# Optimization experiments

Hardware: AMD Instinct MI355X
Metric: run time of the kernel (lower is better)

The kernel has to match this reference:

```python
import jax, jax.numpy as jnp
import numpy as np

B, S = 64, 256
VOCAB, DL, DA, DV = 30522, 300, 74, 35
DH, GH, LH, RH = 128, 64, 128, 128  # modality dim, proj-GRU hidden, LSTM hidden, RGN hidden


def _gru_dir(x, Wi, Wh, bi, bh):
    # x: [B,S,D] -> [B,S,H]; torch GRU gate order (r, z, n)
    xg = x @ Wi + bi  # [B,S,3H] precomputed input projections
    H = Wh.shape[0]
    def step(h, xg_t):
        hg = h @ Wh + bh
        xr, xz, xn = jnp.split(xg_t, 3, axis=-1)
        hr, hz, hn = jnp.split(hg, 3, axis=-1)
        r = jax.nn.sigmoid(xr + hr)
        z = jax.nn.sigmoid(xz + hz)
        n = jnp.tanh(xn + r * hn)
        h = (1.0 - z) * n + z * h
        return h, h
    h0 = jnp.zeros((x.shape[0], H), x.dtype)
    _, ys = jax.lax.scan(step, h0, jnp.swapaxes(xg, 0, 1))
    return jnp.swapaxes(ys, 0, 1)


def _bigru(x, Wi, Wh, bi, bh):
    f = _gru_dir(x, Wi[0], Wh[0], bi[0], bh[0])
    b = _gru_dir(x[:, ::-1], Wi[1], Wh[1], bi[1], bh[1])[:, ::-1]
    return jnp.concatenate([f, b], axis=-1)


def _lstm_dir(x, Wi, Wh, bi, bh):
    xg = x @ Wi + bi  # [B,S,4H]; torch LSTM gate order (i, f, g, o)
    H = Wh.shape[0]
    def step(carry, xg_t):
        h, c = carry
        g = xg_t + h @ Wh + bh
        i, f, gg, o = jnp.split(g, 4, axis=-1)
        c = jax.nn.sigmoid(f) * c + jax.nn.sigmoid(i) * jnp.tanh(gg)
        h = jax.nn.sigmoid(o) * jnp.tanh(c)
        return (h, c), h
    z = jnp.zeros((x.shape[0], H), x.dtype)
    _, ys = jax.lax.scan(step, (z, z), jnp.swapaxes(xg, 0, 1))
    return jnp.swapaxes(ys, 0, 1)


def _bilstm(x, Wi, Wh, bi, bh):
    f = _lstm_dir(x, Wi[0], Wh[0], bi[0], bh[0])
    b = _lstm_dir(x[:, ::-1], Wi[1], Wh[1], bi[1], bh[1])[:, ::-1]
    return jnp.concatenate([f, b], axis=-1)


def _rgn_scan(x, h0, Wx, Wh, b):
    # RGNCell: gated recurrent cell (GRU-style), returns final state [B,H]
    xg = x @ Wx + b  # [B,S,3H]
    def step(h, xg_t):
        hg = h @ Wh
        xr, xz, xn = jnp.split(xg_t, 3, axis=-1)
        hr, hz, hn = jnp.split(hg, 3, axis=-1)
        r = jax.nn.sigmoid(xr + hr)
        z = jax.nn.sigmoid(xz + hz)
        n = jnp.tanh(xn + r * hn)
        return (1.0 - z) * n + z * h, None
    h, _ = jax.lax.scan(step, h0, jnp.swapaxes(xg, 0, 1))
    return h


def _xattn(q, kv):
    # parameter-free scaled dot-product cross-modal attention (JCAF)
    scale = 1.0 / np.sqrt(q.shape[-1]).astype(np.float32)
    s = jnp.einsum('bsd,btd->bst', q, kv) * scale
    return jnp.einsum('bst,btd->bsd', jax.nn.softmax(s, axis=-1), kv)


def _forward(sentences, acoustic, video, state0, state1, emb,
             proj_l_W, proj_l_b, proj_a_W, proj_a_b, proj_v_W, proj_v_b,
             gru_Wi, gru_Wh, gru_bi, gru_bh,
             lstm_Wi, lstm_Wh, lstm_bi, lstm_bh,
             rgn_Wx, rgn_Wh, rgn_b, fc1_W, fc1_b, fc2_W, fc2_b):
    enc = emb[sentences]                          # LanguageEmbeddingLayer: [B,S,DL]
    # SeqEncoder: project each modality to 128-d (dropout off in eval)
    seq_l = enc @ proj_l_W + proj_l_b             # [B,S,128]
    seq_a = acoustic @ proj_a_W + proj_a_b
    seq_v = video @ proj_v_W + proj_v_b
    # project_l/a/v: bidirectional GRU 128 -> 2*64 = 128
    x_l = _bigru(seq_l, gru_Wi[0], gru_Wh[0], gru_bi[0], gru_bh[0])
    x_a = _bigru(seq_a, gru_Wi[1], gru_Wh[1], gru_bi[1], gru_bh[1])
    x_v = _bigru(seq_v, gru_Wi[2], gru_Wh[2], gru_bi[2], gru_bh[2])
    # JCAF: each modality enriched by cross-attention to the other two
    fin_txt = x_l + _xattn(x_l, x_a) + _xattn(x_l, x_v)
    fin_aud = x_a + _xattn(x_a, x_l) + _xattn(x_a, x_v)
    fin_vis = x_v + _xattn(x_v, x_l) + _xattn(x_v, x_a)
    tstep = jnp.concatenate([fin_txt, fin_aud, fin_vis], axis=-1)      # [B,S,384]
    step_fusion = _bilstm(tstep, lstm_Wi, lstm_Wh, lstm_bi, lstm_bh)   # [B,S,256]
    # two custom RGNCell recurrences: forward sweep + reversed sweep
    out0 = _rgn_scan(step_fusion, state0, rgn_Wx[0], rgn_Wh[0], rgn_b[0])
    out1 = _rgn_scan(step_fusion[:, ::-1], state1, rgn_Wx[1], rgn_Wh[1], rgn_b[1])
    h = jax.nn.leaky_relu((out0 + out1) @ fc1_W + fc1_b)
    return h @ fc2_W + fc2_b                     # [B,1]


def setup_inputs():
    keys = iter(jax.random.split(jax.random.key(0), 48))
    def rn(shape, s=0.05):
        return jax.random.normal(next(keys), shape, jnp.float32) * s
    return {
        'sentences': jax.random.randint(next(keys), (B, S), 0, VOCAB),
        'acoustic': jax.random.normal(next(keys), (B, S, DA), jnp.float32),
        'video': jax.random.normal(next(keys), (B, S, DV), jnp.float32),
        'state0': jax.random.normal(next(keys), (B, RH), jnp.float32),
        'state1': jax.random.normal(next(keys), (B, RH), jnp.float32),
        'emb': rn((VOCAB, DL), 0.1),
        'proj_l_W': rn((DL, DH)), 'proj_l_b': rn((DH,)),
        'proj_a_W': rn((DA, DH)), 'proj_a_b': rn((DH,)),
        'proj_v_W': rn((DV, DH)), 'proj_v_b': rn((DH,)),
        'gru_Wi': rn((3, 2, DH, 3 * GH)), 'gru_Wh': rn((3, 2, GH, 3 * GH)),
        'gru_bi': rn((3, 2, 3 * GH)), 'gru_bh': rn((3, 2, 3 * GH)),
        'lstm_Wi': rn((2, 3 * DH, 4 * LH)), 'lstm_Wh': rn((2, LH, 4 * LH)),
        'lstm_bi': rn((2, 4 * LH)), 'lstm_bh': rn((2, 4 * LH)),
        'rgn_Wx': rn((2, 2 * LH, 3 * RH)), 'rgn_Wh': rn((2, RH, 3 * RH)),
        'rgn_b': rn((2, 3 * RH)),
        'fc1_W': rn((RH, 32)), 'fc1_b': rn((32,)),
        'fc2_W': rn((32, 1)), 'fc2_b': rn((1,)),
    }


def reference(sentences, acoustic, video, state0, state1, emb,
              proj_l_W, proj_l_b, proj_a_W, proj_a_b, proj_v_W, proj_v_b,
              gru_Wi, gru_Wh, gru_bi, gru_bh,
              lstm_Wi, lstm_Wh, lstm_bi, lstm_bh,
              rgn_Wx, rgn_Wh, rgn_b, fc1_W, fc1_b, fc2_W, fc2_b):
    return _forward(sentences, acoustic, video, state0, state1, emb,
                    proj_l_W, proj_l_b, proj_a_W, proj_a_b, proj_v_W, proj_v_b,
                    gru_Wi, gru_Wh, gru_bi, gru_bh,
                    lstm_Wi, lstm_Wh, lstm_bi, lstm_bh,
                    rgn_Wx, rgn_Wh, rgn_b, fc1_W, fc1_b, fc2_W, fc2_b)
```

## Files before the change

### kernel.cpp

```cpp
#include <hip/hip_runtime.h>

#define WS_SEQ      0LL
#define WS_XGGRU    6291456LL
#define WS_X        0LL
#define WS_TSTEP    18874368LL
#define WS_S        6291456LL
#define WS_XGLSTM   0LL
#define WS_SF       16777216LL
#define WS_XGRGN    0LL
#define WS_OUT0     20971520LL

__device__ __forceinline__ float sigf(float x) {
    return __builtin_amdgcn_rcpf(1.f + __expf(-x));
}
__device__ __forceinline__ float tanhfast(float x) {
    float e = __expf(2.f * x);
    return 1.f - 2.f * __builtin_amdgcn_rcpf(e + 1.f);
}
__device__ __forceinline__ float rl(float v, int i) {
    return __int_as_float(__builtin_amdgcn_readlane(__float_as_int(v), i));
}

typedef float vf16 __attribute__((ext_vector_type(16)));

#define LD16(V, P, S) { _Pragma("unroll") \
    for (int _j = 0; _j < 16; ++_j) (V)[_j] = (P)[_j * (S)]; }
#define DOT16(ACC, V, H, B) { _Pragma("unroll") \
    for (int _j = 0; _j < 16; ++_j) (ACC) = fmaf(rl((H), (B) + _j), (V)[_j], (ACC)); }

__device__ __forceinline__ void gemm_body(
    const float* __restrict__ Ab, int lda, const int* __restrict__ idx,
    const float* __restrict__ Wb, int wld, int wtrans,
    const float* __restrict__ bb,
    float* __restrict__ Cb, int ldc,
    int K, float alpha, int accum)
{
    int m0 = blockIdx.y * 64, n0 = blockIdx.x * 64;
    int t = threadIdx.x;
    int tx = t & 7, ty = t >> 3;

    __shared__ __align__(16) float As[16][68];
    __shared__ __align__(16) float Ws[16][68];

    float acc[8][8];
#pragma unroll
    for (int i = 0; i < 8; ++i)
#pragma unroll
        for (int j = 0; j < 8; ++j) acc[i][j] = 0.f;

    long long arow[4];
#pragma unroll
    for (int i = 0; i < 4; ++i) {
        int m = (t + i * 64) >> 2;
        arow[i] = idx ? (long long)idx[m0 + m] : (long long)(m0 + m);
    }
    const bool a_vec = ((lda & 3) == 0);

    for (int k0 = 0; k0 < K; k0 += 16) {
#pragma unroll
        for (int i = 0; i < 4; ++i) {
            int j = t + i * 64;
            int m = j >> 2, kq = j & 3;
            int kk = k0 + kq * 4;
            const float* p = Ab + arow[i] * (long long)lda + kk;
            float4 v = {0.f, 0.f, 0.f, 0.f};
            if (a_vec && kk + 3 < K) {
                v = *(const float4*)p;
            } else {
                if (kk + 0 < K) v.x = p[0];
                if (kk + 1 < K) v.y = p[1];
                if (kk + 2 < K) v.z = p[2];
                if (kk + 3 < K) v.w = p[3];
            }
            As[kq * 4 + 0][m] = v.x; As[kq * 4 + 1][m] = v.y;
            As[kq * 4 + 2][m] = v.z; As[kq * 4 + 3][m] = v.w;
        }
        if (!wtrans) {
#pragma unroll
            for (int i = 0; i < 4; ++i) {
                int j = t + i * 64;
                int k = j >> 4, nq = j & 15;
                float4 v = {0.f, 0.f, 0.f, 0.f};
                if (k0 + k < K)
                    v = *(const float4*)(Wb + (long long)(k0 + k) * wld + n0 + nq * 4);
                *(float4*)&Ws[k][nq * 4] = v;
            }
        } else {
#pragma unroll
            for (int i = 0; i < 4; ++i) {
                int j = t + i * 64;
                int n = j >> 2, kq = j & 3;
                int kk = k0 + kq * 4;
                const float* p = Wb + (long long)(n0 + n) * wld + kk;
                float4 v = {0.f, 0.f, 0.f, 0.f};
                if (kk + 3 < K) v = *(const float4*)p;
                else {
                    if (kk + 0 < K) v.x = p[0];
                    if (kk + 1 < K) v.y = p[1];
                    if (kk + 2 < K) v.z = p[2];
                    if (kk + 3 < K) v.w = p[3];
                }
                Ws[kq * 4 + 0][n] = v.x; Ws[kq * 4 + 1][n] = v.y;
                Ws[kq * 4 + 2][n] = v.z; Ws[kq * 4 + 3][n] = v.w;
            }
        }
        __syncthreads();
#pragma unroll
        for (int k = 0; k < 16; ++k) {
            float4 a0 = *(const float4*)&As[k][ty * 8];
            float4 a1 = *(const float4*)&As[k][ty * 8 + 4];
            float4 b0 = *(const float4*)&Ws[k][tx * 8];
            float4 b1 = *(const float4*)&Ws[k][tx * 8 + 4];
            float av[8] = {a0.x, a0.y, a0.z, a0.w, a1.x, a1.y, a1.z, a1.w};
            float bv[8] = {b0.x, b0.y, b0.z, b0.w, b1.x, b1.y, b1.z, b1.w};
#pragma unroll
            for (int i = 0; i < 8; ++i)
#pragma unroll
                for (int j = 0; j < 8; ++j)
                    acc[i][j] = fmaf(av[i], bv[j], acc[i][j]);
        }
        __syncthreads();
    }

#pragma unroll
    for (int i = 0; i < 8; ++i) {
        long long gm = m0 + ty * 8 + i;
#pragma unroll
        for (int jq = 0; jq < 2; ++jq) {
            float* cp = Cb + gm * ldc + n0 + tx * 8 + jq * 4;
            float4 v;
            v.x = alpha * acc[i][jq * 4 + 0]; v.y = alpha * acc[i][jq * 4 + 1];
            v.z = alpha * acc[i][jq * 4 + 2]; v.w = alpha * acc[i][jq * 4 + 3];
            if (bb) {
                const float* bp = bb + n0 + tx * 8 + jq * 4;
                v.x += bp[0]; v.y += bp[1]; v.z += bp[2]; v.w += bp[3];
            }
            if (accum) {
                float4 o = *(const float4*)cp;
                v.x += o.x; v.y += o.y; v.z += o.z; v.w += o.w;
            }
            *(float4*)cp = v;
        }
    }
}

__global__ __launch_bounds__(64) void gemm_k(
    const float* __restrict__ A, long long a_z, int a_zdiv, int lda,
    const int* __restrict__ idx,
    const float* __restrict__ W, long long w_z, int wld, int wtrans,
    const float* __restrict__ bias, int bias_z,
    float* __restrict__ C, long long c_z, int ldc,
    int K, float alpha, int accum)
{
    int z = blockIdx.z;
    gemm_body(A + (long long)(z / a_zdiv) * a_z, lda, idx,
              W + (long long)z * w_z, wld, wtrans,
              bias ? bias + (long long)z * bias_z : nullptr,
              C + (long long)z * c_z, ldc, K, alpha, accum);
}

__global__ __launch_bounds__(64) void att_score_k(
    const float* __restrict__ X, float* __restrict__ S,
    int q0, int q1, int q2, int k0, int k1, int k2)
{
    int z = blockIdx.z;
    int pair = z >> 6, b = z & 63;
    int qi = pair == 0 ? q0 : (pair == 1 ? q1 : q2);
    int ki = pair == 0 ? k0 : (pair == 1 ? k1 : k2);
    gemm_body(X + (long long)qi * 2097152 + (long long)b * 32768, 128, nullptr,
              X + (long long)ki * 2097152 + (long long)b * 32768, 128, 1,
              nullptr,
              S + (long long)z * 65536, 256, 128, 0.08838834764831845f, 0);
}

__global__ __launch_bounds__(64) void att_apply_k(
    const float* __restrict__ S, const float* __restrict__ X,
    float* __restrict__ tstep,
    int q0, int q1, int q2, int k0, int k1, int k2)
{
    int z = blockIdx.z;
    int pair = z >> 6, b = z & 63;
    int qi = pair == 0 ? q0 : (pair == 1 ? q1 : q2);
    int ki = pair == 0 ? k0 : (pair == 1 ? k1 : k2);
    gemm_body(S + (long long)z * 65536, 256, nullptr,
              X + (long long)ki * 2097152 + (long long)b * 32768, 128, 0,
              nullptr,
              tstep + (long long)qi * 128 + (long long)b * 98304, 384,
              256, 1.f, 1);
}

__global__ __launch_bounds__(256) void copy_tstep_k(const float* __restrict__ x,
                                                    float* __restrict__ tstep)
{
    int o = blockIdx.x * 256 + threadIdx.x;
    int c = o % 384;
    int row = o / 384;
    int m = c >> 7, cc = c & 127;
    tstep[o] = x[(long long)m * 2097152 + (long long)row * 128 + cc];
}

__global__ __launch_bounds__(256) void softmax_k(float* __restrict__ S)
{
    int wave = threadIdx.x >> 6, lane = threadIdx.x & 63;
    int row = blockIdx.x * 4 + wave;
    float* p = S + (long long)row * 256;
    float v[4];
    float mx = -1e30f;
#pragma unroll
    for (int i = 0; i < 4; ++i) { v[i] = p[lane + i * 64]; mx = fmaxf(mx, v[i]); }
#pragma unroll
    for (int off = 32; off > 0; off >>= 1) mx = fmaxf(mx, __shfl_xor(mx, off));
    float sum = 0.f;
#pragma unroll
    for (int i = 0; i < 4; ++i) { v[i] = __expf(v[i] - mx); sum += v[i]; }
#pragma unroll
    for (int off = 32; off > 0; off >>= 1) sum += __shfl_xor(sum, off);
    float inv = 1.f / sum;
#pragma unroll
    for (int i = 0; i < 4; ++i) p[lane + i * 64] = v[i] * inv;
}

__global__ __launch_bounds__(192) void gru_rec_k(const float* __restrict__ xg,
                                                 const float* __restrict__ Wh,
                                                 const float* __restrict__ bh,
                                                 float* __restrict__ xout)
{
    int b = blockIdx.x, z = blockIdx.y;
    int m = z >> 1, d = z & 1;
    int tid = threadIdx.x, lane = tid & 63;
    int c = tid;
    const float* Whz = Wh + (long long)z * 12288;
    const float* wp = Whz + c;
    vf16 W0, W1, W2, W3;
    LD16(W0, wp + 0 * 16 * 192, 192); LD16(W1, wp + 1 * 16 * 192, 192);
    LD16(W2, wp + 2 * 16 * 192, 192); LD16(W3, wp + 3 * 16 * 192, 192);
    float bias = bh[z * 192 + c];

    __shared__ float g[2][192];
    int n = lane;
    float h = 0.f;
    const float* xgb = xg + (long long)z * 3145728 + (long long)b * 49152;
    float* xob = xout + (long long)m * 2097152 + (long long)b * 32768 + d * 64;
    int tt0 = d ? 255 : 0;
    const float* xr0 = xgb + tt0 * 192;
    float x_r = xr0[n], x_z = xr0[64 + n], x_n = xr0[128 + n];

#pragma unroll 1
    for (int t = 0; t < 256; ++t) {
        int tt = d ? 255 - t : t;
        float nx_r = 0, nx_z = 0, nx_n = 0;
        if (t < 255) {
            const float* xr = xgb + (d ? tt - 1 : tt + 1) * 192;
            nx_r = xr[n]; nx_z = xr[64 + n]; nx_n = xr[128 + n];
        }
        float s0 = bias, s1 = 0.f, s2 = 0.f, s3 = 0.f;
        DOT16(s0, W0, h, 0);  DOT16(s1, W1, h, 16);
        DOT16(s2, W2, h, 32); DOT16(s3, W3, h, 48);
        g[t & 1][c] = (s0 + s1) + (s2 + s3);
        __syncthreads();
        const float* gp = g[t & 1];
        float r  = sigf(x_r + gp[n]);
        float zz = sigf(x_z + gp[64 + n]);
        float nn = tanhfast(x_n + r * gp[128 + n]);
        h = (1.f - zz) * nn + zz * h;
        if (c < 64) xob[tt * 128 + n] = h;
        x_r = nx_r; x_z = nx_z; x_n = nx_n;
    }
}

__global__ __launch_bounds__(1024) void lstm_rec_k(const float* __restrict__ xg,
                                                   const float* __restrict__ Wh,
                                                   const float* __restrict__ bh,
                                                   float* __restrict__ sf)
{
    int b = blockIdx.x, d = blockIdx.y;
    int tid = threadIdx.x, lane = tid & 63;
    int kh = tid >> 9;
    int c  = tid & 511;
    const float* Whz = Wh + (long long)d * 65536;
    const float* wp = Whz + (long long)(kh * 64) * 512 + c;
    vf16 W0, W1, W2, W3;
    LD16(W0, wp + 0 * 16 * 512, 512); LD16(W1, wp + 1 * 16 * 512, 512);
    LD16(W2, wp + 2 * 16 * 512, 512); LD16(W3, wp + 3 * 16 * 512, 512);

    __shared__ float part[2][1024];
    int n = kh * 64 + lane;
    float h = 0.f, cst = 0.f;
    const float* xgb = xg + (long long)d * 8388608 + (long long)b * 131072;
    float* sfb = sf + (long long)b * 65536 + d * 128;

    float bias = 0.f, xc = 0.f;
    if (kh == 0) {
        bias = bh[d * 512 + c];
        int tt0 = d ? 255 : 0;
        xc = xgb[tt0 * 512 + c];
    }

#pragma unroll 1
    for (int t = 0; t < 256; ++t) {
        int tt = d ? 255 - t : t;
        float nxc = 0.f;
        if (kh == 0 && t < 255)
            nxc = xgb[(d ? tt - 1 : tt + 1) * 512 + c];
        float s0 = xc + bias, s1 = 0.f, s2 = 0.f, s3 = 0.f;
        DOT16(s0, W0, h, 0);  DOT16(s1, W1, h, 16);
        DOT16(s2, W2, h, 32); DOT16(s3, W3, h, 48);
        part[t & 1][kh * 512 + c] = (s0 + s1) + (s2 + s3);
        __syncthreads();
        const float* p = part[t & 1];
        float iv = p[n]       + p[512 + n];
        float fv = p[128 + n] + p[512 + 128 + n];
        float gv = p[256 + n] + p[512 + 256 + n];
        float ov = p[384 + n] + p[512 + 384 + n];
        cst = sigf(fv) * cst + sigf(iv) * tanhfast(gv);
        h = sigf(ov) * tanhfast(cst);
        if (c < 64) sfb[tt * 256 + n] = h;
        xc = nxc;
    }
}

__global__ __launch_bounds__(768) void rgn_rec_k(const float* __restrict__ xg,
                                                 const float* __restrict__ Wh,
                                                 const float* __restrict__ state0,
                                                 const float* __restrict__ state1,
                                                 float* __restrict__ outbase)
{
    int b = blockIdx.x, d = blockIdx.y;
    int tid = threadIdx.x, lane = tid & 63;
    int kh = (tid >= 384) ? 1 : 0;
    int c  = tid - kh * 384;
    const float* Whz = Wh + (long long)d * 49152;
    const float* wp = Whz + (long long)(kh * 64) * 384 + c;
    vf16 W0, W1, W2, W3;
    LD16(W0, wp + 0 * 16 * 384, 384); LD16(W1, wp + 1 * 16 * 384, 384);
    LD16(W2, wp + 2 * 16 * 384, 384); LD16(W3, wp + 3 * 16 * 384, 384);

    __shared__ float part[2][768];
    int n = kh * 64 + lane;
    const float* st = d ? state1 : state0;
    float h = st[b * 128 + n];
    const float* xgb = xg + (long long)d * 6291456 + (long long)b * 98304;
    int tt0 = d ? 255 : 0;
    const float* xr0 = xgb + tt0 * 384;
    float x_r = xr0[n], x_z = xr0[128 + n], x_n = xr0[256 + n];

#pragma unroll 1
    for (int t = 0; t < 256; ++t) {
        int tt = d ? 255 - t : t;
        float nx_r = 0, nx_z = 0, nx_n = 0;
        if (t < 255) {
            const float* xr = xgb + (d ? tt - 1 : tt + 1) * 384;
            nx_r = xr[n]; nx_z = xr[128 + n]; nx_n = xr[256 + n];
        }
        float s0 = 0.f, s1 = 0.f, s2 = 0.f, s3 = 0.f;
        DOT16(s0, W0, h, 0);  DOT16(s1, W1, h, 16);
        DOT16(s2, W2, h, 32); DOT16(s3, W3, h, 48);
        part[t & 1][kh * 384 + c] = (s0 + s1) + (s2 + s3);
        __syncthreads();
        const float* p = part[t & 1];
        float pr = p[n]       + p[384 + n];
        float pz = p[128 + n] + p[384 + 128 + n];
        float pn = p[256 + n] + p[384 + 256 + n];
        float r  = sigf(x_r + pr);
        float zz = sigf(x_z + pz);
        float nn = tanhfast(x_n + r * pn);
        h = (1.f - zz) * nn + zz * h;
        x_r = nx_r; x_z = nx_z; x_n = nx_n;
    }
    if (c < 64) outbase[(long long)d * 8192 + b * 128 + n] = h;
}

__global__ __launch_bounds__(256) void fc_k(const float* __restrict__ o01,
                                            const float* __restrict__ f1W,
                                            const float* __restrict__ f1b,
                                            const float* __restrict__ f2W,
                                            const float* __restrict__ f2b,
                                            float* __restrict__ out)
{
    __shared__ float s[8192];
    __shared__ float h1[2048];
    int tid = threadIdx.x;
    for (int e = tid; e < 8192; e += 256) s[e] = o01[e] + o01[8192 + e];
    __syncthreads();
    for (int o = tid; o < 2048; o += 256) {
        int b = o >> 5, q = o & 31;
        float acc = f1b[q];
        for (int k = 0; k < 128; ++k) acc += s[b * 128 + k] * f1W[k * 32 + q];
        h1[o] = acc >= 0.f ? acc : 0.01f * acc;
    }
    __syncthreads();
    if (tid < 64) {
        float acc = f2b[0];
        for (int q = 0; q < 32; ++q) acc += h1[tid * 32 + q] * f2W[q];
        out[tid] = acc;
    }
}

extern "C" void kernel_launch(void* const* d_in, const int* in_sizes, int n_in,
                              void* d_out, int out_size, void* d_ws, size_t ws_size,
                              hipStream_t stream)
{
    const int*   sent     = (const int*)  d_in[0];
    const float* acoustic = (const float*)d_in[1];
    const float* video    = (const float*)d_in[2];
    const float* state0   = (const float*)d_in[3];
    const float* state1   = (const float*)d_in[4];
    const float* emb      = (const float*)d_in[5];
    const float* plW = (const float*)d_in[6],  *plb = (const float*)d_in[7];
    const float* paW = (const float*)d_in[8],  *pab = (const float*)d_in[9];
    const float* pvW = (const float*)d_in[10], *pvb = (const float*)d_in[11];
    const float* gWi = (const float*)d_in[12], *gWh = (const float*)d_in[13];
    const float* gbi = (const float*)d_in[14], *gbh = (const float*)d_in[15];
    const float* lWi = (const float*)d_in[16], *lWh = (const float*)d_in[17];
    const float* lbi = (const float*)d_in[18], *lbh = (const float*)d_in[19];
    const float* rWx = (const float*)d_in[20], *rWh = (const float*)d_in[21];
    const float* rb  = (const float*)d_in[22];
    const float* f1W = (const float*)d_in[23], *f1b = (const float*)d_in[24];
    const float* f2W = (const float*)d_in[25], *f2b = (const float*)d_in[26];
    float* ws  = (float*)d_ws;
    float* out = (float*)d_out;

    dim3 blk(64);

    gemm_k<<<dim3(2, 256, 1), blk, 0, stream>>>(emb, 0, 1, 300, sent,
        plW, 0, 128, 0, plb, 0, ws + WS_SEQ, 0, 128, 300, 1.f, 0);
    gemm_k<<<dim3(2, 256, 1), blk, 0, stream>>>(acoustic, 0, 1, 74, nullptr,
        paW, 0, 128, 0, pab, 0, ws + WS_SEQ + 2097152, 0, 128, 74, 1.f, 0);
    gemm_k<<<dim3(2, 256, 1), blk, 0, stream>>>(video, 0, 1, 35, nullptr,
        pvW, 0, 128, 0, pvb, 0, ws + WS_SEQ + 4194304, 0, 128, 35, 1.f, 0);

    gemm_k<<<dim3(3, 256, 6), blk, 0, stream>>>(ws + WS_SEQ, 2097152, 2, 128, nullptr,
        gWi, 24576, 192, 0, gbi, 192, ws + WS_XGGRU, 3145728, 192, 128, 1.f, 0);

    gru_rec_k<<<dim3(64, 6), dim3(192), 0, stream>>>(ws + WS_XGGRU, gWh, gbh, ws + WS_X);

    copy_tstep_k<<<dim3(24576), dim3(256), 0, stream>>>(ws + WS_X, ws + WS_TSTEP);

    att_score_k<<<dim3(4, 4, 192), blk, 0, stream>>>(ws + WS_X, ws + WS_S,
        0, 1, 2, 1, 0, 0);
    softmax_k<<<dim3(12288), dim3(256), 0, stream>>>(ws + WS_S);
    att_apply_k<<<dim3(2, 4, 192), blk, 0, stream>>>(ws + WS_S, ws + WS_X,
        ws + WS_TSTEP, 0, 1, 2, 1, 0, 0);
    att_score_k<<<dim3(4, 4, 192), blk, 0, stream>>>(ws + WS_X, ws + WS_S,
        0, 1, 2, 2, 2, 1);
    softmax_k<<<dim3(12288), dim3(256), 0, stream>>>(ws + WS_S);
    att_apply_k<<<dim3(2, 4, 192), blk, 0, stream>>>(ws + WS_S, ws + WS_X,
        ws + WS_TSTEP, 0, 1, 2, 2, 2, 1);

    gemm_k<<<dim3(8, 256, 2), blk, 0, stream>>>(ws + WS_TSTEP, 0, 1, 384, nullptr,
        lWi, 196608, 512, 0, lbi, 512, ws + WS_XGLSTM, 8388608, 512, 384, 1.f, 0);

    lstm_rec_k<<<dim3(64, 2), dim3(1024), 0, stream>>>(ws + WS_XGLSTM, lWh, lbh, ws + WS_SF);

    gemm_k<<<dim3(6, 256, 2), blk, 0, stream>>>(ws + WS_SF, 0, 1, 256, nullptr,
        rWx, 98304, 384, 0, rb, 384, ws + WS_XGRGN, 6291456, 384, 256, 1.f, 0);

    rgn_rec_k<<<dim3(64, 2), dim3(768), 0, stream>>>(ws + WS_XGRGN, rWh, state0, state1,
                                                     ws + WS_OUT0);

    fc_k<<<dim3(1), dim3(256), 0, stream>>>(ws + WS_OUT0, f1W, f1b, f2W, f2b, out);
}
```

Baseline: 1.654 ms.

## Use packed FP32 FMA in recurrent kernels with two output columns per thread

The GRU, LSTM and RGN recurrence kernels now give each thread two adjacent gate columns. They hold the weights as 64 float2 registers and run the hidden-state matvec with inline-asm v_pk_fma_f32, using readlane-broadcast hidden values placed in hardcoded SGPR pairs. Block sizes are halved (192→128, 1024→512, 768→384), which cuts the number of waves and FMA instructions per serial timestep. The cost is extra readlane and s_mov instructions plus hand-pinned scalar registers. In the GRU, part of a wave now sits idle during the matvec.

```diff
diff --git a/kernel.cpp b/kernel.cpp
--- a/kernel.cpp
+++ b/kernel.cpp
@@ -17,16 +17,46 @@
     float e = __expf(2.f * x);
     return 1.f - 2.f * __builtin_amdgcn_rcpf(e + 1.f);
 }
-__device__ __forceinline__ float rl(float v, int i) {
-    return __int_as_float(__builtin_amdgcn_readlane(__float_as_int(v), i));
-}
-
-typedef float vf16 __attribute__((ext_vector_type(16)));
-
-#define LD16(V, P, S) { _Pragma("unroll") \
-    for (int _j = 0; _j < 16; ++_j) (V)[_j] = (P)[_j * (S)]; }
-#define DOT16(ACC, V, H, B) { _Pragma("unroll") \
-    for (int _j = 0; _j < 16; ++_j) (ACC) = fmaf(rl((H), (B) + _j), (V)[_j], (ACC)); }
+
+typedef float vf2 __attribute__((ext_vector_type(2)));
+
+#define LDW64(W, P, S) { _Pragma("unroll") \
+    for (int _k = 0; _k < 64; ++_k) (W)[_k] = *(const vf2*)((P) + _k * (S)); }
+
+#define PK4(A0, A1, Wa, Wb, Wc, Wd, H, K0, K1, K2, K3) \
+  asm("v_readlane_b32 s60, %6, " #K0 "\n\t" \
+      "v_readlane_b32 s62, %6, " #K1 "\n\t" \
+      "v_readlane_b32 s64, %6, " #K2 "\n\t" \
+      "v_readlane_b32 s66, %6, " #K3 "\n\t" \
+      "s_mov_b32 s61, s60\n\t" \
+      "s_mov_b32 s63, s62\n\t" \
+      "s_mov_b32 s65, s64\n\t" \
+      "s_mov_b32 s67, s66\n\t" \
+      "v_pk_fma_f32 %0, %2, s[60:61], %0\n\t" \
+      "v_pk_fma_f32 %1, %3, s[62:63], %1\n\t" \
+      "v_pk_fma_f32 %0, %4, s[64:65], %0\n\t" \
+      "v_pk_fma_f32 %1, %5, s[66:67], %1" \
+      : "+v"(A0), "+v"(A1) \
+      : "v"(Wa), "v"(Wb), "v"(Wc), "v"(Wd), "v"(H) \
+      : "s60","s61","s62","s63","s64","s65","s66","s67");
+
+#define PKALL(A0, A1, W, H) \
+  PK4(A0,A1,W[0],W[1],W[2],W[3],H,0,1,2,3) \
+  PK4(A0,A1,W[4],W[5],W[6],W[7],H,4,5,6,7) \
+  PK4(A0,A1,W[8],W[9],W[10],W[11],H,8,9,10,11) \
+  PK4(A0,A1,W[12],W[13],W[14],W[15],H,12,13,14,15) \
+  PK4(A0,A1,W[16],W[17],W[18],W[19],H,16,17,18,19) \
+  PK4(A0,A1,W[20],W[21],W[22],W[23],H,20,21,22,23) \
+  PK4(A0,A1,W[24],W[25],W[26],W[27],H,24,25,26,27) \
+  PK4(A0,A1,W[28],W[29],W[30],W[31],H,28,29,30,31) \
+  PK4(A0,A1,W[32],W[33],W[34],W[35],H,32,33,34,35) \
+  PK4(A0,A1,W[36],W[37],W[38],W[39],H,36,37,38,39) \
+  PK4(A0,A1,W[40],W[41],W[42],W[43],H,40,41,42,43) \
+  PK4(A0,A1,W[44],W[45],W[46],W[47],H,44,45,46,47) \
+  PK4(A0,A1,W[48],W[49],W[50],W[51],H,48,49,50,51) \
+  PK4(A0,A1,W[52],W[53],W[54],W[55],H,52,53,54,55) \
+  PK4(A0,A1,W[56],W[57],W[58],W[59],H,56,57,58,59) \
+  PK4(A0,A1,W[60],W[61],W[62],W[63],H,60,61,62,63)
 
 __device__ __forceinline__ void gemm_body(
     const float* __restrict__ Ab, int lda, const int* __restrict__ idx,
@@ -220,7 +250,7 @@
     for (int i = 0; i < 4; ++i) p[lane + i * 64] = v[i] * inv;
 }
 
-__global__ __launch_bounds__(192) void gru_rec_k(const float* __restrict__ xg,
+__global__ __launch_bounds__(128) void gru_rec_k(const float* __restrict__ xg,
                                                  const float* __restrict__ Wh,
                                                  const float* __restrict__ bh,
                                                  float* __restrict__ xout)
@@ -228,13 +258,14 @@
     int b = blockIdx.x, z = blockIdx.y;
     int m = z >> 1, d = z & 1;
     int tid = threadIdx.x, lane = tid & 63;
-    int c = tid;
+    int cp = tid;
+    int act = cp < 96;
+    int cpc = act ? cp : 0;
     const float* Whz = Wh + (long long)z * 12288;
-    const float* wp = Whz + c;
-    vf16 W0, W1, W2, W3;
-    LD16(W0, wp + 0 * 16 * 192, 192); LD16(W1, wp + 1 * 16 * 192, 192);
-    LD16(W2, wp + 2 * 16 * 192, 192); LD16(W3, wp + 3 * 16 * 192, 192);
-    float bias = bh[z * 192 + c];
+    const float* wp = Whz + 2 * cpc;
+    vf2 Wk[64];
+    LDW64(Wk, wp, 192);
+    vf2 bias2 = *(const vf2*)(bh + z * 192 + 2 * cpc);
 
     __shared__ float g[2][192];
     int n = lane;
@@ -253,35 +284,33 @@
             const float* xr = xgb + (d ? tt - 1 : tt + 1) * 192;
             nx_r = xr[n]; nx_z = xr[64 + n]; nx_n = xr[128 + n];
         }
-        float s0 = bias, s1 = 0.f, s2 = 0.f, s3 = 0.f;
-        DOT16(s0, W0, h, 0);  DOT16(s1, W1, h, 16);
-        DOT16(s2, W2, h, 32); DOT16(s3, W3, h, 48);
-        g[t & 1][c] = (s0 + s1) + (s2 + s3);
+        vf2 a0 = bias2, a1 = {0.f, 0.f};
+        PKALL(a0, a1, Wk, h);
+        if (act) *(vf2*)&g[t & 1][2 * cp] = a0 + a1;
         __syncthreads();
         const float* gp = g[t & 1];
         float r  = sigf(x_r + gp[n]);
         float zz = sigf(x_z + gp[64 + n]);
         float nn = tanhfast(x_n + r * gp[128 + n]);
         h = (1.f - zz) * nn + zz * h;
-        if (c < 64) xob[tt * 128 + n] = h;
+        if (tid < 64) xob[tt * 128 + n] = h;
         x_r = nx_r; x_z = nx_z; x_n = nx_n;
     }
 }
 
-__global__ __launch_bounds__(1024) void lstm_rec_k(const float* __restrict__ xg,
-                                                   const float* __restrict__ Wh,
-                                                   const float* __restrict__ bh,
-                                                   float* __restrict__ sf)
+__global__ __launch_bounds__(512) void lstm_rec_k(const float* __restrict__ xg,
+                                                  const float* __restrict__ Wh,
+                                                  const float* __restrict__ bh,
+                                                  float* __restrict__ sf)
 {
     int b = blockIdx.x, d = blockIdx.y;
     int tid = threadIdx.x, lane = tid & 63;
-    int kh = tid >> 9;
-    int c  = tid & 511;
+    int kh = tid >> 8;
+    int cp = tid & 255;
     const float* Whz = Wh + (long long)d * 65536;
-    const float* wp = Whz + (long long)(kh * 64) * 512 + c;
-    vf16 W0, W1, W2, W3;
-    LD16(W0, wp + 0 * 16 * 512, 512); LD16(W1, wp + 1 * 16 * 512, 512);
-    LD16(W2, wp + 2 * 16 * 512, 512); LD16(W3, wp + 3 * 16 * 512, 512);
+    const float* wp = Whz + (long long)(kh * 64) * 512 + 2 * cp;
+    vf2 Wk[64];
+    LDW64(Wk, wp, 512);
 
     __shared__ float part[2][1024];
     int n = kh * 64 + lane;
@@ -289,23 +318,22 @@
     const float* xgb = xg + (long long)d * 8388608 + (long long)b * 131072;
     float* sfb = sf + (long long)b * 65536 + d * 128;
 
-    float bias = 0.f, xc = 0.f;
+    vf2 bias2 = {0.f, 0.f}, xc2 = {0.f, 0.f};
     if (kh == 0) {
-        bias = bh[d * 512 + c];
+        bias2 = *(const vf2*)(bh + d * 512 + 2 * cp);
         int tt0 = d ? 255 : 0;
-        xc = xgb[tt0 * 512 + c];
+        xc2 = *(const vf2*)(xgb + tt0 * 512 + 2 * cp);
     }
 
 #pragma unroll 1
     for (int t = 0; t < 256; ++t) {
         int tt = d ? 255 - t : t;
-        float nxc = 0.f;
+        vf2 nxc2 = {0.f, 0.f};
         if (kh == 0 && t < 255)
-            nxc = xgb[(d ? tt - 1 : tt + 1) * 512 + c];
-        float s0 = xc + bias, s1 = 0.f, s2 = 0.f, s3 = 0.f;
-        DOT16(s0, W0, h, 0);  DOT16(s1, W1, h, 16);
-        DOT16(s2, W2, h, 32); DOT16(s3, W3, h, 48);
-        part[t & 1][kh * 512 + c] = (s0 + s1) + (s2 + s3);
+            nxc2 = *(const vf2*)(xgb + (d ? tt - 1 : tt + 1) * 512 + 2 * cp);
+        vf2 a0 = xc2 + bias2, a1 = {0.f, 0.f};
+        PKALL(a0, a1, Wk, h);
+        *(vf2*)&part[t & 1][kh * 512 + 2 * cp] = a0 + a1;
         __syncthreads();
         const float* p = part[t & 1];
         float iv = p[n]       + p[512 + n];
@@ -314,12 +342,12 @@
         float ov = p[384 + n] + p[512 + 384 + n];
         cst = sigf(fv) * cst + sigf(iv) * tanhfast(gv);
         h = sigf(ov) * tanhfast(cst);
-        if (c < 64) sfb[tt * 256 + n] = h;
-        xc = nxc;
-    }
-}
-
-__global__ __launch_bounds__(768) void rgn_rec_k(const float* __restrict__ xg,
+        if (cp < 64) sfb[tt * 256 + n] = h;
+        xc2 = nxc2;
+    }
+}
+
+__global__ __launch_bounds__(384) void rgn_rec_k(const float* __restrict__ xg,
                                                  const float* __restrict__ Wh,
                                                  const float* __restrict__ state0,
                                                  const float* __restrict__ state1,
@@ -327,13 +355,12 @@
 {
     int b = blockIdx.x, d = blockIdx.y;
     int tid = threadIdx.x, lane = tid & 63;
-    int kh = (tid >= 384) ? 1 : 0;
-    int c  = tid - kh * 384;
+    int kh = (tid >= 192) ? 1 : 0;
+    int cp = tid - kh * 192;
     const float* Whz = Wh + (long long)d * 49152;
-    const float* wp = Whz + (long long)(kh * 64) * 384 + c;
-    vf16 W0, W1, W2, W3;
-    LD16(W0, wp + 0 * 16 * 384, 384); LD16(W1, wp + 1 * 16 * 384, 384);
-    LD16(W2, wp + 2 * 16 * 384, 384); LD16(W3, wp + 3 * 16 * 384, 384);
+    const float* wp = Whz + (long long)(kh * 64) * 384 + 2 * cp;
+    vf2 Wk[64];
+    LDW64(Wk, wp, 384);
 
     __shared__ float part[2][768];
     int n = kh * 64 + lane;
@@ -352,10 +379,9 @@
             const float* xr = xgb + (d ? tt - 1 : tt + 1) * 384;
             nx_r = xr[n]; nx_z = xr[128 + n]; nx_n = xr[256 + n];
         }
-        float s0 = 0.f, s1 = 0.f, s2 = 0.f, s3 = 0.f;
-        DOT16(s0, W0, h, 0);  DOT16(s1, W1, h, 16);
-        DOT16(s2, W2, h, 32); DOT16(s3, W3, h, 48);
-        part[t & 1][kh * 384 + c] = (s0 + s1) + (s2 + s3);
+        vf2 a0 = {0.f, 0.f}, a1 = {0.f, 0.f};
+        PKALL(a0, a1, Wk, h);
+        *(vf2*)&part[t & 1][kh * 384 + 2 * cp] = a0 + a1;
         __syncthreads();
         const float* p = part[t & 1];
         float pr = p[n]       + p[384 + n];
@@ -367,7 +393,7 @@
         h = (1.f - zz) * nn + zz * h;
         x_r = nx_r; x_z = nx_z; x_n = nx_n;
     }
-    if (c < 64) outbase[(long long)d * 8192 + b * 128 + n] = h;
+    if (cp < 64) outbase[(long long)d * 8192 + b * 128 + n] = h;
 }
 
 __global__ __launch_bounds__(256) void fc_k(const float* __restrict__ o01,
@@ -432,7 +458,7 @@
     gemm_k<<<dim3(3, 256, 6), blk, 0, stream>>>(ws + WS_SEQ, 2097152, 2, 128, nullptr,
         gWi, 24576, 192, 0, gbi, 192, ws + WS_XGGRU, 3145728, 192, 128, 1.f, 0);
 
-    gru_rec_k<<<dim3(64, 6), dim3(192), 0, stream>>>(ws + WS_XGGRU, gWh, gbh, ws + WS_X);
+    gru_rec_k<<<dim3(64, 6), dim3(128), 0, stream>>>(ws + WS_XGGRU, gWh, gbh, ws + WS_X);
 
     copy_tstep_k<<<dim3(24576), dim3(256), 0, stream>>>(ws + WS_X, ws + WS_TSTEP);
 
@@ -450,12 +476,12 @@
     gemm_k<<<dim3(8, 256, 2), blk, 0, stream>>>(ws + WS_TSTEP, 0, 1, 384, nullptr,
         lWi, 196608, 512, 0, lbi, 512, ws + WS_XGLSTM, 8388608, 512, 384, 1.f, 0);
 
-    lstm_rec_k<<<dim3(64, 2), dim3(1024), 0, stream>>>(ws + WS_XGLSTM, lWh, lbh, ws + WS_SF);
+    lstm_rec_k<<<dim3(64, 2), dim3(512), 0, stream>>>(ws + WS_XGLSTM, lWh, lbh, ws + WS_SF);
 
     gemm_k<<<dim3(6, 256, 2), blk, 0, stream>>>(ws + WS_SF, 0, 1, 256, nullptr,
         rWx, 98304, 384, 0, rb, 384, ws + WS_XGRGN, 6291456, 384, 256, 1.f, 0);
 
-    rgn_rec_k<<<dim3(64, 2), dim3(768), 0, stream>>>(ws + WS_XGRGN, rWh, state0, state1,
+    rgn_rec_k<<<dim3(64, 2), dim3(384), 0, stream>>>(ws + WS_XGRGN, rWh, state0, state1,
                                                      ws + WS_OUT0);
 
     fc_k<<<dim3(1), dim3(256), 0, stream>>>(ws + WS_OUT0, f1W, f1b, f2W, f2b, out);
```

Result: slower. 1.729 ms (+4.5%).

## Widen GEMM tiles to 64x128 with packed FMA and restructure LSTM recurrence

Applied to the files above, without the earlier changes.

The shared GEMM body now computes 64x128 output tiles per 64-thread block, accumulating with two-wide vector FMAs (packed FP32). A new N bound masks the partial column tiles, and launch bounds are tightened to one block. The LSTM recurrence kernel is halved to 512 threads, each handling two gate columns. Part of the recurrent weight matrix (36 rows) is staged in LDS, and the other 28 rows are read from global memory each step. This aims to cut register pressure and use packed math, at the cost of more accumulator registers in the GEMM and global weight traffic on every recurrence step.

```diff
diff --git a/kernel.cpp b/kernel.cpp
--- a/kernel.cpp
+++ b/kernel.cpp
@@ -22,6 +22,7 @@
 }
 
 typedef float vf16 __attribute__((ext_vector_type(16)));
+typedef float vf2 __attribute__((ext_vector_type(2)));
 
 #define LD16(V, P, S) { _Pragma("unroll") \
     for (int _j = 0; _j < 16; ++_j) (V)[_j] = (P)[_j * (S)]; }
@@ -33,20 +34,20 @@
     const float* __restrict__ Wb, int wld, int wtrans,
     const float* __restrict__ bb,
     float* __restrict__ Cb, int ldc,
-    int K, float alpha, int accum)
-{
-    int m0 = blockIdx.y * 64, n0 = blockIdx.x * 64;
+    int K, int N, float alpha, int accum)
+{
+    int m0 = blockIdx.y * 64, n0 = blockIdx.x * 128;
     int t = threadIdx.x;
     int tx = t & 7, ty = t >> 3;
 
     __shared__ __align__(16) float As[16][68];
-    __shared__ __align__(16) float Ws[16][68];
-
-    float acc[8][8];
+    __shared__ __align__(16) float Ws[16][132];
+
+    vf2 acc2[8][8];
 #pragma unroll
     for (int i = 0; i < 8; ++i)
 #pragma unroll
-        for (int j = 0; j < 8; ++j) acc[i][j] = 0.f;
+        for (int p = 0; p < 8; ++p) acc2[i][p] = (vf2){0.f, 0.f};
 
     long long arow[4];
 #pragma unroll
@@ -77,28 +78,31 @@
         }
         if (!wtrans) {
 #pragma unroll
-            for (int i = 0; i < 4; ++i) {
-                int j = t + i * 64;
-                int k = j >> 4, nq = j & 15;
+            for (int i = 0; i < 8; ++i) {
+                int q = t + i * 64;
+                int k = q >> 5, nq = q & 31;
+                int col = n0 + nq * 4;
                 float4 v = {0.f, 0.f, 0.f, 0.f};
-                if (k0 + k < K)
-                    v = *(const float4*)(Wb + (long long)(k0 + k) * wld + n0 + nq * 4);
+                if (k0 + k < K && col < N)
+                    v = *(const float4*)(Wb + (long long)(k0 + k) * wld + col);
                 *(float4*)&Ws[k][nq * 4] = v;
             }
         } else {
 #pragma unroll
-            for (int i = 0; i < 4; ++i) {
-                int j = t + i * 64;
-                int n = j >> 2, kq = j & 3;
+            for (int i = 0; i < 8; ++i) {
+                int q = t + i * 64;
+                int n = q >> 2, kq = q & 3;
                 int kk = k0 + kq * 4;
-                const float* p = Wb + (long long)(n0 + n) * wld + kk;
                 float4 v = {0.f, 0.f, 0.f, 0.f};
-                if (kk + 3 < K) v = *(const float4*)p;
-                else {
-                    if (kk + 0 < K) v.x = p[0];
-                    if (kk + 1 < K) v.y = p[1];
-                    if (kk + 2 < K) v.z = p[2];
-                    if (kk + 3 < K) v.w = p[3];
+                if (n0 + n < N) {
+                    const float* p = Wb + (long long)(n0 + n) * wld + kk;
+                    if (kk + 3 < K) v = *(const float4*)p;
+                    else {
+                        if (kk + 0 < K) v.x = p[0];
+                        if (kk + 1 < K) v.y = p[1];
+                        if (kk + 2 < K) v.z = p[2];
+                        if (kk + 3 < K) v.w = p[3];
+                    }
                 }
                 Ws[kq * 4 + 0][n] = v.x; Ws[kq * 4 + 1][n] = v.y;
                 Ws[kq * 4 + 2][n] = v.z; Ws[kq * 4 + 3][n] = v.w;
@@ -109,15 +113,23 @@
         for (int k = 0; k < 16; ++k) {
             float4 a0 = *(const float4*)&As[k][ty * 8];
             float4 a1 = *(const float4*)&As[k][ty * 8 + 4];
-            float4 b0 = *(const float4*)&Ws[k][tx * 8];
-            float4 b1 = *(const float4*)&Ws[k][tx * 8 + 4];
+            float4 b0 = *(const float4*)&Ws[k][tx * 4];
+            float4 b1 = *(const float4*)&Ws[k][32 + tx * 4];
+            float4 b2 = *(const float4*)&Ws[k][64 + tx * 4];
+            float4 b3 = *(const float4*)&Ws[k][96 + tx * 4];
             float av[8] = {a0.x, a0.y, a0.z, a0.w, a1.x, a1.y, a1.z, a1.w};
-            float bv[8] = {b0.x, b0.y, b0.z, b0.w, b1.x, b1.y, b1.z, b1.w};
-#pragma unroll
-            for (int i = 0; i < 8; ++i)
-#pragma unroll
-                for (int j = 0; j < 8; ++j)
-                    acc[i][j] = fmaf(av[i], bv[j], acc[i][j]);
+            vf2 bv[8];
+            bv[0] = (vf2){b0.x, b0.y}; bv[1] = (vf2){b0.z, b0.w};
+            bv[2] = (vf2){b1.x, b1.y}; bv[3] = (vf2){b1.z, b1.w};
+            bv[4] = (vf2){b2.x, b2.y}; bv[5] = (vf2){b2.z, b2.w};
+            bv[6] = (vf2){b3.x, b3.y}; bv[7] = (vf2){b3.z, b3.w};
+#pragma unroll
+            for (int i = 0; i < 8; ++i) {
+                vf2 a2 = {av[i], av[i]};
+#pragma unroll
+                for (int p = 0; p < 8; ++p)
+                    acc2[i][p] = __builtin_elementwise_fma(a2, bv[p], acc2[i][p]);
+            }
         }
         __syncthreads();
     }
@@ -126,40 +138,45 @@
     for (int i = 0; i < 8; ++i) {
         long long gm = m0 + ty * 8 + i;
 #pragma unroll
-        for (int jq = 0; jq < 2; ++jq) {
-            float* cp = Cb + gm * ldc + n0 + tx * 8 + jq * 4;
-            float4 v;
-            v.x = alpha * acc[i][jq * 4 + 0]; v.y = alpha * acc[i][jq * 4 + 1];
-            v.z = alpha * acc[i][jq * 4 + 2]; v.w = alpha * acc[i][jq * 4 + 3];
-            if (bb) {
-                const float* bp = bb + n0 + tx * 8 + jq * 4;
-                v.x += bp[0]; v.y += bp[1]; v.z += bp[2]; v.w += bp[3];
+        for (int jj = 0; jj < 4; ++jj) {
+            int col = n0 + jj * 32 + tx * 4;
+            if (col < N) {
+                float* cp = Cb + gm * ldc + col;
+                float4 v;
+                v.x = alpha * acc2[i][jj * 2 + 0][0];
+                v.y = alpha * acc2[i][jj * 2 + 0][1];
+                v.z = alpha * acc2[i][jj * 2 + 1][0];
+                v.w = alpha * acc2[i][jj * 2 + 1][1];
+                if (bb) {
+                    const float* bp = bb + col;
+                    v.x += bp[0]; v.y += bp[1]; v.z += bp[2]; v.w += bp[3];
+                }
+                if (accum) {
+                    float4 o = *(const float4*)cp;
+                    v.x += o.x; v.y += o.y; v.z += o.z; v.w += o.w;
+                }
+                *(float4*)cp = v;
             }
-            if (accum) {
-                float4 o = *(const float4*)cp;
-                v.x += o.x; v.y += o.y; v.z += o.z; v.w += o.w;
-            }
-            *(float4*)cp = v;
-        }
-    }
-}
-
-__global__ __launch_bounds__(64) void gemm_k(
+        }
+    }
+}
+
+__global__ __launch_bounds__(64, 1) void gemm_k(
     const float* __restrict__ A, long long a_z, int a_zdiv, int lda,
     const int* __restrict__ idx,
     const float* __restrict__ W, long long w_z, int wld, int wtrans,
     const float* __restrict__ bias, int bias_z,
     float* __restrict__ C, long long c_z, int ldc,
-    int K, float alpha, int accum)
+    int K, int N, float alpha, int accum)
 {
     int z = blockIdx.z;
     gemm_body(A + (long long)(z / a_zdiv) * a_z, lda, idx,
               W + (long long)z * w_z, wld, wtrans,
               bias ? bias + (long long)z * bias_z : nullptr,
-              C + (long long)z * c_z, ldc, K, alpha, accum);
-}
-
-__global__ __launch_bounds__(64) void att_score_k(
+              C + (long long)z * c_z, ldc, K, N, alpha, accum);
+}
+
+__global__ __launch_bounds__(64, 1) void att_score_k(
     const float* __restrict__ X, float* __restrict__ S,
     int q0, int q1, int q2, int k0, int k1, int k2)
 {
@@ -170,10 +187,10 @@
     gemm_body(X + (long long)qi * 2097152 + (long long)b * 32768, 128, nullptr,
               X + (long long)ki * 2097152 + (long long)b * 32768, 128, 1,
               nullptr,
-              S + (long long)z * 65536, 256, 128, 0.08838834764831845f, 0);
-}
-
-__global__ __launch_bounds__(64) void att_apply_k(
+              S + (long long)z * 65536, 256, 128, 256, 0.08838834764831845f, 0);
+}
+
+__global__ __launch_bounds__(64, 1) void att_apply_k(
     const float* __restrict__ S, const float* __restrict__ X,
     float* __restrict__ tstep,
     int q0, int q1, int q2, int k0, int k1, int k2)
@@ -186,7 +203,7 @@
               X + (long long)ki * 2097152 + (long long)b * 32768, 128, 0,
               nullptr,
               tstep + (long long)qi * 128 + (long long)b * 98304, 384,
-              256, 1.f, 1);
+              256, 128, 1.f, 1);
 }
 
 __global__ __launch_bounds__(256) void copy_tstep_k(const float* __restrict__ x,
@@ -268,44 +285,64 @@
     }
 }
 
-__global__ __launch_bounds__(1024) void lstm_rec_k(const float* __restrict__ xg,
-                                                   const float* __restrict__ Wh,
-                                                   const float* __restrict__ bh,
-                                                   float* __restrict__ sf)
+__global__ __launch_bounds__(512) void lstm_rec_k(const float* __restrict__ xg,
+                                                  const float* __restrict__ Wh,
+                                                  const float* __restrict__ bh,
+                                                  float* __restrict__ sf)
 {
     int b = blockIdx.x, d = blockIdx.y;
     int tid = threadIdx.x, lane = tid & 63;
-    int kh = tid >> 9;
-    int c  = tid & 511;
+    int kh = tid >> 8;
+    int cp = tid & 255;
     const float* Whz = Wh + (long long)d * 65536;
-    const float* wp = Whz + (long long)(kh * 64) * 512 + c;
-    vf16 W0, W1, W2, W3;
-    LD16(W0, wp + 0 * 16 * 512, 512); LD16(W1, wp + 1 * 16 * 512, 512);
-    LD16(W2, wp + 2 * 16 * 512, 512); LD16(W3, wp + 3 * 16 * 512, 512);
-
+
+    __shared__ __align__(16) float wlds[36864];
     __shared__ float part[2][1024];
+    for (int i = tid; i < 9216; i += 512) {
+        int row = i >> 7, c4 = (i & 127) << 2;
+        int srow = row < 36 ? row : row + 28;
+        *(float4*)&wlds[row * 512 + c4] = *(const float4*)(Whz + srow * 512 + c4);
+    }
+    const float* wl  = wlds + (kh * 36) * 512 + 2 * cp;
+    const float* wpg = Whz + (long long)(kh * 64 + 36) * 512 + 2 * cp;
+
     int n = kh * 64 + lane;
     float h = 0.f, cst = 0.f;
     const float* xgb = xg + (long long)d * 8388608 + (long long)b * 131072;
     float* sfb = sf + (long long)b * 65536 + d * 128;
 
-    float bias = 0.f, xc = 0.f;
+    vf2 bias2 = {0.f, 0.f}, xc2 = {0.f, 0.f};
     if (kh == 0) {
-        bias = bh[d * 512 + c];
+        bias2 = *(const vf2*)(bh + d * 512 + 2 * cp);
         int tt0 = d ? 255 : 0;
-        xc = xgb[tt0 * 512 + c];
-    }
+        xc2 = *(const vf2*)(xgb + tt0 * 512 + 2 * cp);
+    }
+    __syncthreads();
 
 #pragma unroll 1
     for (int t = 0; t < 256; ++t) {
         int tt = d ? 255 - t : t;
-        float nxc = 0.f;
+        vf2 nxc2 = {0.f, 0.f};
         if (kh == 0 && t < 255)
-            nxc = xgb[(d ? tt - 1 : tt + 1) * 512 + c];
-        float s0 = xc + bias, s1 = 0.f, s2 = 0.f, s3 = 0.f;
-        DOT16(s0, W0, h, 0);  DOT16(s1, W1, h, 16);
-        DOT16(s2, W2, h, 32); DOT16(s3, W3, h, 48);
-        part[t & 1][kh * 512 + c] = (s0 + s1) + (s2 + s3);
+            nxc2 = *(const vf2*)(xgb + (d ? tt - 1 : tt + 1) * 512 + 2 * cp);
+        vf2 a0 = xc2 + bias2, a1 = {0.f, 0.f};
+#pragma unroll
+        for (int r = 0; r < 36; ++r) {
+            float hs = rl(h, r);
+            vf2 hb = {hs, hs};
+            vf2 w = *(const vf2*)(wl + r * 512);
+            if (r & 1) a1 = __builtin_elementwise_fma(hb, w, a1);
+            else       a0 = __builtin_elementwise_fma(hb, w, a0);
+        }
+#pragma unroll
+        for (int r = 0; r < 28; ++r) {
+            float hs = rl(h, 36 + r);
+            vf2 hb = {hs, hs};
+            vf2 w = *(const vf2*)(wpg + r * 512);
+            if (r & 1) a1 = __builtin_elementwise_fma(hb, w, a1);
+            else       a0 = __builtin_elementwise_fma(hb, w, a0);
+        }
+        *(vf2*)&part[t & 1][kh * 512 + 2 * cp] = a0 + a1;
         __syncthreads();
         const float* p = part[t & 1];
         float iv = p[n]       + p[512 + n];
@@ -314,8 +351,8 @@
         float ov = p[384 + n] + p[512 + 384 + n];
         cst = sigf(fv) * cst + sigf(iv) * tanhfast(gv);
         h = sigf(ov) * tanhfast(cst);
-        if (c < 64) sfb[tt * 256 + n] = h;
-        xc = nxc;
+        if (cp < 64) sfb[tt * 256 + n] = h;
+        xc2 = nxc2;
     }
 }
 
@@ -422,38 +459,38 @@
 
     dim3 blk(64);
 
-    gemm_k<<<dim3(2, 256, 1), blk, 0, stream>>>(emb, 0, 1, 300, sent,
-        plW, 0, 128, 0, plb, 0, ws + WS_SEQ, 0, 128, 300, 1.f, 0);
-    gemm_k<<<dim3(2, 256, 1), blk, 0, stream>>>(acoustic, 0, 1, 74, nullptr,
-        paW, 0, 128, 0, pab, 0, ws + WS_SEQ + 2097152, 0, 128, 74, 1.f, 0);
-    gemm_k<<<dim3(2, 256, 1), blk, 0, stream>>>(video, 0, 1, 35, nullptr,
-        pvW, 0, 128, 0, pvb, 0, ws + WS_SEQ + 4194304, 0, 128, 35, 1.f, 0);
-
-    gemm_k<<<dim3(3, 256, 6), blk, 0, stream>>>(ws + WS_SEQ, 2097152, 2, 128, nullptr,
-        gWi, 24576, 192, 0, gbi, 192, ws + WS_XGGRU, 3145728, 192, 128, 1.f, 0);
+    gemm_k<<<dim3(1, 256, 1), blk, 0, stream>>>(emb, 0, 1, 300, sent,
+        plW, 0, 128, 0, plb, 0, ws + WS_SEQ, 0, 128, 300, 128, 1.f, 0);
+    gemm_k<<<dim3(1, 256, 1), blk, 0, stream>>>(acoustic, 0, 1, 74, nullptr,
+        paW, 0, 128, 0, pab, 0, ws + WS_SEQ + 2097152, 0, 128, 74, 128, 1.f, 0);
+    gemm_k<<<dim3(1, 256, 1), blk, 0, stream>>>(video, 0, 1, 35, nullptr,
+        pvW, 0, 128, 0, pvb, 0, ws + WS_SEQ + 4194304, 0, 128, 35, 128, 1.f, 0);
+
+    gemm_k<<<dim3(2, 256, 6), blk, 0, stream>>>(ws + WS_SEQ, 2097152, 2, 128, nullptr,
+        gWi, 24576, 192, 0, gbi, 192, ws + WS_XGGRU, 3145728, 192, 128, 192, 1.f, 0);
 
     gru_rec_k<<<dim3(64, 6), dim3(192), 0, stream>>>(ws + WS_XGGRU, gWh, gbh, ws + WS_X);
 
     copy_tstep_k<<<dim3(24576), dim3(256), 0, stream>>>(ws + WS_X, ws + WS_TSTEP);
 
-    att_score_k<<<dim3(4, 4, 192), blk, 0, stream>>>(ws + WS_X, ws + WS_S,
+    att_score_k<<<dim3(2, 4, 192), blk, 0, stream>>>(ws + WS_X, ws + WS_S,
         0, 1, 2, 1, 0, 0);
     softmax_k<<<dim3(12288), dim3(256), 0, stream>>>(ws + WS_S);
-    att_apply_k<<<dim3(2, 4, 192), blk, 0, stream>>>(ws + WS_S, ws + WS_X,
+    att_apply_k<<<dim3(1, 4, 192), blk, 0, stream>>>(ws + WS_S, ws + WS_X,
         ws + WS_TSTEP, 0, 1, 2, 1, 0, 0);
-    att_score_k<<<dim3(4, 4, 192), blk, 0, stream>>>(ws + WS_X, ws + WS_S,
+    att_score_k<<<dim3(2, 4, 192), blk, 0, stream>>>(ws + WS_X, ws + WS_S,
         0, 1, 2, 2, 2, 1);
     softmax_k<<<dim3(12288), dim3(256), 0, stream>>>(ws + WS_S);
-    att_apply_k<<<dim3(2, 4, 192), blk, 0, stream>>>(ws + WS_S, ws + WS_X,
+    att_apply_k<<<dim3(1, 4, 192), blk, 0, stream>>>(ws + WS_S, ws + WS_X,
         ws + WS_TSTEP, 0, 1, 2, 2, 2, 1);
 
-    gemm_k<<<dim3(8, 256, 2), blk, 0, stream>>>(ws + WS_TSTEP, 0, 1, 384, nullptr,
-        lWi, 196608, 512, 0, lbi, 512, ws + WS_XGLSTM, 8388608, 512, 384, 1.f, 0);
-
-    lstm_rec_k<<<dim3(64, 2), dim3(1024), 0, stream>>>(ws + WS_XGLSTM, lWh, lbh, ws + WS_SF);
-
-    gemm_k<<<dim3(6, 256, 2), blk, 0, stream>>>(ws + WS_SF, 0, 1, 256, nullptr,
-        rWx, 98304, 384, 0, rb, 384, ws + WS_XGRGN, 6291456, 384, 256, 1.f, 0);
+    gemm_k<<<dim3(4, 256, 2), blk, 0, stream>>>(ws + WS_TSTEP, 0, 1, 384, nullptr,
+        lWi, 196608, 512, 0, lbi, 512, ws + WS_XGLSTM, 8388608, 512, 384, 512, 1.f, 0);
+
+    lstm_rec_k<<<dim3(64, 2), dim3(512), 0, stream>>>(ws + WS_XGLSTM, lWh, lbh, ws + WS_SF);
+
+    gemm_k<<<dim3(3, 256, 2), blk, 0, stream>>>(ws + WS_SF, 0, 1, 256, nullptr,
+        rWx, 98304, 384, 0, rb, 384, ws + WS_XGRGN, 6291456, 384, 256, 384, 1.f, 0);
 
     rgn_rec_k<<<dim3(64, 2), dim3(768), 0, stream>>>(ws + WS_XGRGN, rWh, state0, state1,
                                                      ws + WS_OUT0);
```

Measured after the change: 1.716 ms. 3.7% more time.
